# Kernel tuning notes

Measured on AMD Instinct MI355X. Metric: run time of the kernel, lower is better.

## Reference

```python
import jax, jax.numpy as jnp
import numpy as np

N_NODES = 50000
N_EDGES = 1000000
IN_CH = 128
OUT_CH = 128
N_HEADS = 8
CIS = 8.0


def _edge_conv(x, e, wq, bq, wk, bk, wv, bv, n_heads, cis):
    """One EdgeConv layer (PyG mean aggregation, source_to_target flow)."""
    src, dst = e[0], e[1]                       # x_j = x[src], x_i = x[dst]
    xi = x[dst]
    xj = x[src]
    feat = jnp.concatenate([xi, xj - xi], axis=1)        # [E, 2C]
    q = feat @ wq + bq                                   # [E, O]
    k = feat @ wk + bk
    v = feat @ wv + bv
    E, O = q.shape
    hs = O // n_heads
    q = q.reshape(E, n_heads, hs)
    k = k.reshape(E, n_heads, hs)
    v = v.reshape(E, n_heads, hs)
    # edge_weight = sign(log|dst-src| - log(cis))
    d = jnp.abs(dst - src).astype(q.dtype)
    ew = jnp.sign(jnp.log(d) - jnp.log(jnp.asarray(cis, q.dtype)))
    v = v * ew[:, None, None]
    scale = jnp.asarray(1.0 / np.sqrt(hs), q.dtype)
    probs = jax.nn.softmax(q * k * scale, axis=-1)       # softmax over head_size
    ctx = (probs * v).reshape(E, O)                      # [E, O]
    n = x.shape[0]
    s = jax.ops.segment_sum(ctx, dst, num_segments=n)    # mean aggr over targets
    cnt = jax.ops.segment_sum(jnp.ones((E,), ctx.dtype), dst, num_segments=n)
    return s / jnp.maximum(cnt, 1.0)[:, None]


def setup_inputs() -> dict:
    key = jax.random.key(0)
    ks = jax.random.split(key, 24)
    x = jax.random.normal(ks[0], (N_NODES, IN_CH), jnp.float32)
    edge_index = jax.random.randint(ks[1], (2, N_EDGES), 0, N_NODES, dtype=jnp.int32)
    half = N_EDGES // 2
    e0 = edge_index[:, jax.random.permutation(ks[2], N_EDGES)[:half]]
    e1 = edge_index[:, jax.random.permutation(ks[3], N_EDGES)[:half]]
    e2 = edge_index[:, jax.random.permutation(ks[4], N_EDGES)[:half]]
    batch = jnp.zeros((N_NODES,), jnp.int32)

    def mk(k, i, o):
        return jax.random.normal(k, (i, o), jnp.float32) * 0.02

    def mkb(k, o):
        return jax.random.normal(k, (o,), jnp.float32) * 0.02

    # layer dims: conv0 128->128, conv1 128->64, conv2 64->128
    return dict(
        x=x, e0=e0, e1=e1, e2=e2, batch=batch,
        wq0=mk(ks[5], 2 * IN_CH, OUT_CH), bq0=mkb(ks[6], OUT_CH),
        wk0=mk(ks[7], 2 * IN_CH, OUT_CH), bk0=mkb(ks[8], OUT_CH),
        wv0=mk(ks[9], 2 * IN_CH, OUT_CH), bv0=mkb(ks[10], OUT_CH),
        wq1=mk(ks[11], 2 * OUT_CH, OUT_CH // 2), bq1=mkb(ks[12], OUT_CH // 2),
        wk1=mk(ks[13], 2 * OUT_CH, OUT_CH // 2), bk1=mkb(ks[14], OUT_CH // 2),
        wv1=mk(ks[15], 2 * OUT_CH, OUT_CH // 2), bv1=mkb(ks[16], OUT_CH // 2),
        wq2=mk(ks[17], OUT_CH, OUT_CH), bq2=mkb(ks[18], OUT_CH),
        wk2=mk(ks[19], OUT_CH, OUT_CH), bk2=mkb(ks[20], OUT_CH),
        wv2=mk(ks[21], OUT_CH, OUT_CH), bv2=mkb(ks[22], OUT_CH),
    )


def reference(x, e0, e1, e2, batch,
              wq0, bq0, wk0, bk0, wv0, bv0,
              wq1, bq1, wk1, bk1, wv1, bv1,
              wq2, bq2, wk2, bk2, wv2, bv2):
    x0 = jax.nn.relu(_edge_conv(x, e0, wq0, bq0, wk0, bk0, wv0, bv0, N_HEADS, CIS))
    h = jax.nn.relu(_edge_conv(x0, e1, wq1, bq1, wk1, bk1, wv1, bv1, N_HEADS, CIS))
    h = _edge_conv(h, e2, wq2, bq2, wk2, bk2, wv2, bv2, N_HEADS, CIS)
    return jax.nn.relu(h + x0)
```

## Files before the change

### kernel.cpp

```cpp
#include <hip/hip_runtime.h>
#include <hip/hip_fp16.h>


typedef _Float16 f16x8 __attribute__((ext_vector_type(8)));
typedef unsigned int u32x4 __attribute__((ext_vector_type(4)));
typedef float f32x4 __attribute__((ext_vector_type(4)));
typedef float f32x2 __attribute__((ext_vector_type(2)));

__device__ __forceinline__ unsigned short f2h(float f) {
  __half h = __float2half(f);
  return *reinterpret_cast<unsigned short*>(&h);
}
__device__ __forceinline__ __half2 ash2(unsigned w) {
  return *reinterpret_cast<__half2*>(&w);
}

__device__ __forceinline__ void pack_w_seg(const float* __restrict__ wq,
                                           const float* __restrict__ wk,
                                           const float* __restrict__ wv,
                                           unsigned short* __restrict__ dst,
                                           int IN, int O, float kscale, int id) {
  int kchunks = IN >> 5, nchunks = O >> 4;
  int total = 6 * nchunks * kchunks * 64;
  if (id >= total) return;
  int lane = id & 63;
  int frag = id >> 6;
  int kc = frag % kchunks;
  int nc = (frag / kchunks) % nchunks;
  int mat = frag / (kchunks * nchunks);
  const float* w = (mat % 3 == 0) ? wq : (mat % 3 == 1) ? wk : wv;
  float mul = (mat % 3 == 1) ? kscale : 1.0f;
  int n = nc * 16 + (lane & 15);
  int k0 = kc * 32 + (lane >> 4) * 8;
  unsigned short tmp[8];
#pragma unroll
  for (int j = 0; j < 8; ++j) {
    int row = k0 + j;
    float bot = w[(size_t)(IN + row) * O + n];
    float val = (mat < 3) ? (w[(size_t)row * O + n] - bot) : bot;
    tmp[j] = f2h(val * mul);
  }
  uint4 o;
  o.x = (unsigned)tmp[0] | ((unsigned)tmp[1] << 16);
  o.y = (unsigned)tmp[2] | ((unsigned)tmp[3] << 16);
  o.z = (unsigned)tmp[4] | ((unsigned)tmp[5] << 16);
  o.w = (unsigned)tmp[6] | ((unsigned)tmp[7] << 16);
  reinterpret_cast<uint4*>(dst)[id] = o;
}

__device__ __forceinline__ void pack_b_seg(const float* __restrict__ bq,
                                           const float* __restrict__ bk,
                                           const float* __restrict__ bv, float kscale, int O,
                                           float* __restrict__ out, int i) {
  int mat = i / O, c = i % O;
  float v = 0.f;
  if (mat == 0) v = bq[c];
  else if (mat == 1) v = bk[c] * kscale;
  else if (mat == 2) v = bv[c];
  out[i] = v;
}

__global__ void preproc(
    const int* __restrict__ e0, const int* __restrict__ e1, const int* __restrict__ e2,
    int E, int* __restrict__ hist, int* __restrict__ rank, int NP,
    const float* __restrict__ x, unsigned short* __restrict__ xb, int n8,
    const float* __restrict__ wq0, const float* __restrict__ wk0, const float* __restrict__ wv0,
    const float* __restrict__ wq1, const float* __restrict__ wk1, const float* __restrict__ wv1,
    const float* __restrict__ wq2, const float* __restrict__ wk2, const float* __restrict__ wv2,
    unsigned short* __restrict__ wp0, unsigned short* __restrict__ wp1,
    unsigned short* __restrict__ wp2,
    const float* __restrict__ bq0, const float* __restrict__ bk0, const float* __restrict__ bv0,
    const float* __restrict__ bq1, const float* __restrict__ bk1, const float* __restrict__ bv1,
    const float* __restrict__ bq2, const float* __restrict__ bk2, const float* __restrict__ bv2,
    float* __restrict__ bias0, float* __restrict__ bias1, float* __restrict__ bias2,
    float sc16, float sc8) {
  const int tid = blockIdx.x * blockDim.x + threadIdx.x;
  const int stride = gridDim.x * blockDim.x;

  for (int i = tid; i < E; i += stride) {
    rank[i] = atomicAdd(&hist[e0[E + i]], 1);
    rank[(size_t)E + i] = atomicAdd(&hist[NP + e1[E + i]], 1);
    rank[2 * (size_t)E + i] = atomicAdd(&hist[2 * NP + e2[E + i]], 1);
  }

  for (int j = tid; j < n8; j += stride) {
    float4 a = reinterpret_cast<const float4*>(x)[2 * j];
    float4 b = reinterpret_cast<const float4*>(x)[2 * j + 1];
    uint4 o;
    o.x = (unsigned)f2h(a.x) | ((unsigned)f2h(a.y) << 16);
    o.y = (unsigned)f2h(a.z) | ((unsigned)f2h(a.w) << 16);
    o.z = (unsigned)f2h(b.x) | ((unsigned)f2h(b.y) << 16);
    o.w = (unsigned)f2h(b.z) | ((unsigned)f2h(b.w) << 16);
    reinterpret_cast<uint4*>(xb)[j] = o;
  }
  if (tid < 12288) pack_w_seg(wq0, wk0, wv0, wp0, 128, 128, sc16, tid);
  else if (tid < 18432) pack_w_seg(wq1, wk1, wv1, wp1, 128, 64, sc8, tid - 12288);
  else if (tid < 24576) pack_w_seg(wq2, wk2, wv2, wp2, 64, 128, sc16, tid - 18432);
  else if (tid < 24576 + 1920) {
    int i = tid - 24576;
    if (i < 768) pack_b_seg(bq0, bk0, bv0, sc16, 128, bias0, i);
    else if (i < 1152) pack_b_seg(bq1, bk1, bv1, sc8, 64, bias1, i - 768);
    else pack_b_seg(bq2, bk2, bv2, sc16, 128, bias2, i - 1152);
  }
}

__device__ __forceinline__ int block_scan_excl256(int v, int* buf, int t, int* total) {
  buf[t] = v;
  __syncthreads();
#pragma unroll
  for (int off = 1; off < 256; off <<= 1) {
    int add = (t >= off) ? buf[t - off] : 0;
    __syncthreads();
    buf[t] += add;
    __syncthreads();
  }
  int incl = buf[t];
  *total = buf[255];
  __syncthreads();
  return incl - v;
}

__global__ void scan_pass1(const int* __restrict__ hist, int* __restrict__ excl,
                           int* __restrict__ bsum, int n, int NP) {
  __shared__ int buf[256];
  int y = blockIdx.y, t = threadIdx.x;
  int i = blockIdx.x * 256 + t;
  int v = (i < n) ? hist[y * NP + i] : 0;
  int total;
  int ex = block_scan_excl256(v, buf, t, &total);
  if (i < NP) excl[y * NP + i] = ex;
  if (t == 0) bsum[y * 256 + blockIdx.x] = total;
}

__global__ void scan_pass2(int* __restrict__ bsum, int nblk) {
  __shared__ int buf[256];
  int y = blockIdx.y, t = threadIdx.x;
  int v = (t < nblk) ? bsum[y * 256 + t] : 0;
  int total;
  int ex = block_scan_excl256(v, buf, t, &total);
  bsum[y * 256 + t] = ex;
}

__global__ void scatter3(const int* __restrict__ e0, const int* __restrict__ e1,
                         const int* __restrict__ e2, int E, const int* __restrict__ excl,
                         const int* __restrict__ bsum, const int* __restrict__ rank,
                         long long* __restrict__ pairs, int NP,
                         uint4* __restrict__ za, int na, uint4* __restrict__ zb, int nb) {
  int y = blockIdx.y;
  const int* e = (y == 0) ? e0 : (y == 1) ? e1 : e2;
  int i = blockIdx.x * 256 + threadIdx.x;
  if (i < E) {
    int sN = e[i], d = e[E + i];
    int pos = excl[y * NP + d] + bsum[y * 256 + (d >> 8)] + rank[(size_t)y * E + i];
    long long val = ((long long)(unsigned)d << 32) | (unsigned)sN;
    __builtin_nontemporal_store(val, &pairs[(size_t)y * E + pos]);
  }
  const int gid = (blockIdx.y * gridDim.x + blockIdx.x) * 256 + threadIdx.x;
  const int gstride = gridDim.x * gridDim.y * 256;
  const uint4 Z = make_uint4(0u, 0u, 0u, 0u);
  for (int j = gid; j < na; j += gstride) za[j] = Z;
  for (int j = gid; j < nb; j += gstride) zb[j] = Z;
}

template <int IN, int O, int G>
__global__ __launch_bounds__(256, 4) void node_gemm(
    const unsigned short* __restrict__ xb, int N, int NT,
    const unsigned short* __restrict__ wpack, const float* __restrict__ bias6,
    unsigned short* __restrict__ Y1, unsigned short* __restrict__ Y2) {
  constexpr int KC = IN / 32;
  constexpr int NCH = O / 16;
  constexpr int CHR = IN / 8;
  constexpr int CM = CHR - 1;
  __shared__ unsigned short tiles[64 * IN];

  const int chunk = gridDim.x >> 3;
  const int lb = (blockIdx.x & 7) * chunk + (blockIdx.x >> 3);
  if (lb >= NT * G) return;
  const int tile = lb / G;
  const int grp = lb % G;

  const int t = threadIdx.x, w = t >> 6, ln = t & 63;
  const int n0 = tile * 64;

  {
    constexpr int RPI = 64 / CHR;
    constexpr int NI = 16 / RPI;
    const int r_in = ln / CHR, c = ln % CHR;
#pragma unroll
    for (int i = 0; i < NI; ++i) {
      int row = w * 16 + i * RPI + r_in;
      int node = min(n0 + row, N - 1);
      int sc = c ^ (row & CM);
      const unsigned short* g = xb + (size_t)node * IN + sc * 8;
      unsigned short* l = &tiles[(size_t)(w * 16 + i * RPI) * IN];
      __builtin_amdgcn_global_load_lds(
          (const __attribute__((address_space(1))) unsigned int*)g,
          (__attribute__((address_space(3))) unsigned int*)l, 16, 0, 0);
    }
  }
  __syncthreads();

  const int col = ln & 15, quad = ln >> 4;
  const int g0 = grp * 8 + w * 2;

  f32x4 acc[2][4];
#pragma unroll
  for (int cc = 0; cc < 2; ++cc)
#pragma unroll
    for (int m = 0; m < 4; ++m) acc[cc][m] = (f32x4){0.f, 0.f, 0.f, 0.f};

#pragma unroll
  for (int kc = 0; kc < KC; ++kc) {
    f16x8 a[4];
#pragma unroll
    for (int m = 0; m < 4; ++m) {
      int row = m * 16 + col;
      int sc = (kc * 4 + quad) ^ (row & CM);
      a[m] = *reinterpret_cast<const f16x8*>(&tiles[(size_t)row * IN + sc * 8]);
    }
#pragma unroll
    for (int cc = 0; cc < 2; ++cc) {
      const f16x8 b = *reinterpret_cast<const f16x8*>(
          wpack + ((size_t)((g0 + cc) * KC + kc) * 64 + ln) * 8);
#pragma unroll
      for (int m = 0; m < 4; ++m)
        acc[cc][m] = __builtin_amdgcn_mfma_f32_16x16x32_f16(a[m], b, acc[cc][m], 0, 0, 0);
    }
  }

#pragma unroll
  for (int cc = 0; cc < 2; ++cc) {
    int gch = g0 + cc;
    int mat = gch / NCH, ncg = gch % NCH;
    unsigned short* Yp = (mat < 3) ? Y1 : Y2;
    int mo = (mat < 3) ? mat : mat - 3;
    float bv = bias6[gch * 16 + col];
    size_t coloff = (size_t)mo * O + ncg * 16 + col;
#pragma unroll
    for (int m = 0; m < 4; ++m)
#pragma unroll
      for (int r = 0; r < 4; ++r) {
        int node = n0 + m * 16 + quad * 4 + r;
        if (node < N) Yp[(size_t)node * (3 * O) + coloff] = f2h(acc[cc][m][r] + bv);
      }
  }
}

template <int O, int HS>
__global__ __launch_bounds__(512, 6) void edge_attn_kernel(
    const unsigned short* __restrict__ Y1, const unsigned short* __restrict__ Y2,
    const int2* __restrict__ pairs, const int E, float* __restrict__ s) {
  constexpr int NL = HS / 8;
  constexpr int PM = O / 4 - 1;
  __shared__ float ctx[64 * O];
  __shared__ int dstL[64];

  const int chunkB = gridDim.x >> 3;
  const int lb = (blockIdx.x & 7) * chunkB + (blockIdx.x >> 3);
  if (lb * 64 >= E) return;

  const int t = threadIdx.x;
  const int e = t >> 3, head = t & 7;
  const int eG = lb * 64 + e;
  const int eC = min(eG, E - 1);
  const bool valid = eG < E;
  const int2 p = pairs[eC];
  const int sN = p.x, dN = p.y;
  if ((t & 7) == 0) dstL[e] = dN;
  const float dd = fabsf((float)(dN - sN));
  const float ew = (dd > 8.f) ? 1.f : ((dd == 8.f) ? 0.f : -1.f);

  const unsigned short* b1 = Y1 + (size_t)dN * (3 * O) + head * HS;
  const unsigned short* b2 = Y2 + (size_t)sN * (3 * O) + head * HS;

  u32x4 q1[NL], q2[NL], k1[NL], k2[NL], v1[NL], v2[NL];
#pragma unroll
  for (int l = 0; l < NL; ++l) {
    q1[l] = *reinterpret_cast<const u32x4*>(b1 + l * 8);
    q2[l] = *reinterpret_cast<const u32x4*>(b2 + l * 8);
    k1[l] = *reinterpret_cast<const u32x4*>(b1 + O + l * 8);
    k2[l] = *reinterpret_cast<const u32x4*>(b2 + O + l * 8);
    v1[l] = *reinterpret_cast<const u32x4*>(b1 + 2 * O + l * 8);
    v2[l] = *reinterpret_cast<const u32x4*>(b2 + 2 * O + l * 8);
  }

  f32x2 ex2[NL * 4];
  f32x2 sum2 = (f32x2){0.f, 0.f};
#pragma unroll
  for (int l = 0; l < NL; ++l)
#pragma unroll
    for (int d = 0; d < 4; ++d) {
      __half2 qh = __hadd2(ash2(q1[l][d]), ash2(q2[l][d]));
      __half2 kh = __hadd2(ash2(k1[l][d]), ash2(k2[l][d]));
      __half2 qk = __hmul2(qh, kh);
      f32x2 eo;
      eo.x = exp2f(__low2float(qk));
      eo.y = exp2f(__high2float(qk));
      ex2[l * 4 + d] = eo;
      sum2 += eo;
    }
  const float sum = sum2.x + sum2.y;
  const float rs = valid ? (ew / sum) : 0.f;
  const f32x2 rs2 = (f32x2){rs, rs};
#pragma unroll
  for (int l = 0; l < NL; ++l) {
#pragma unroll
    for (int g2 = 0; g2 < 2; ++g2) {
      __half2 va = __hadd2(ash2(v1[l][g2 * 2]), ash2(v2[l][g2 * 2]));
      __half2 vb = __hadd2(ash2(v1[l][g2 * 2 + 1]), ash2(v2[l][g2 * 2 + 1]));
      f32x2 vva = (f32x2){__low2float(va), __high2float(va)};
      f32x2 vvb = (f32x2){__low2float(vb), __high2float(vb)};
      f32x2 oa = ex2[l * 4 + g2 * 2] * rs2 * vva;
      f32x2 ob = ex2[l * 4 + g2 * 2 + 1] * rs2 * vvb;
      f32x4 o = (f32x4){oa.x, oa.y, ob.x, ob.y};
      int g = l * 2 + g2;
      int pch = (g * 8 + head + e) & PM;
      *reinterpret_cast<f32x4*>(&ctx[e * O + pch * 4]) = o;
    }
  }
  __syncthreads();

  {
    constexpr int GRP = 512 / O;
    constexpr int EPT = 64 / GRP;
    const int hs2 = t & 7;
    const int cs = (t >> 3) & (HS - 1);
    const int colA = hs2 * HS + cs;
    const int seg0 = (t / O) * EPT;
    const int inv = (cs >> 2) * 8 + hs2;
    const int js = cs & 3;
    float run = 0.f;
    int runstart = 0;
    int dcur = dstL[seg0];
#pragma unroll
    for (int i = 0; i < EPT; ++i) {
      int ee = seg0 + i;
      int pch = (inv + ee) & PM;
      run += ctx[ee * O + pch * 4 + js];
      int dnext = (i < EPT - 1) ? dstL[ee + 1] : -1;
      if (dnext != dcur) {
        float* addr = &s[(size_t)dcur * O + colA];
        if (runstart > 0 && i < EPT - 1) *addr = run;
        else atomicAdd(addr, run);
        run = 0.f;
        runstart = i + 1;
        dcur = dnext;
      }
    }
  }
}

__global__ void finalize_relu_f32h(float* __restrict__ s, const int* __restrict__ cnt,
                                   unsigned short* __restrict__ xbo, int total4, int Odiv4) {
  int i = blockIdx.x * blockDim.x + threadIdx.x;
  if (i >= total4) return;
  int node = i / Odiv4;
  float c = fmaxf((float)cnt[node], 1.0f);
  float4 v = reinterpret_cast<float4*>(s)[i];
  v.x = fmaxf(v.x / c, 0.f);
  v.y = fmaxf(v.y / c, 0.f);
  v.z = fmaxf(v.z / c, 0.f);
  v.w = fmaxf(v.w / c, 0.f);
  reinterpret_cast<float4*>(s)[i] = v;
  ushort4 o = make_ushort4(f2h(v.x), f2h(v.y), f2h(v.z), f2h(v.w));
  reinterpret_cast<ushort4*>(xbo)[i] = o;
}

__global__ void finalize_relu_h(const float* __restrict__ s, const int* __restrict__ cnt,
                                unsigned short* __restrict__ xbo, int total4, int Odiv4) {
  int i = blockIdx.x * blockDim.x + threadIdx.x;
  if (i >= total4) return;
  int node = i / Odiv4;
  float c = fmaxf((float)cnt[node], 1.0f);
  float4 v = reinterpret_cast<const float4*>(s)[i];
  ushort4 o = make_ushort4(f2h(fmaxf(v.x / c, 0.f)), f2h(fmaxf(v.y / c, 0.f)),
                           f2h(fmaxf(v.z / c, 0.f)), f2h(fmaxf(v.w / c, 0.f)));
  reinterpret_cast<ushort4*>(xbo)[i] = o;
}

__global__ void finalize_add_relu(float* __restrict__ out, const float* __restrict__ x0,
                                  const int* __restrict__ cnt, int total4, int Odiv4) {
  int i = blockIdx.x * blockDim.x + threadIdx.x;
  if (i >= total4) return;
  int node = i / Odiv4;
  float c = fmaxf((float)cnt[node], 1.0f);
  float4 v = reinterpret_cast<float4*>(out)[i];
  float4 r = reinterpret_cast<const float4*>(x0)[i];
  v.x = fmaxf(v.x / c + r.x, 0.f);
  v.y = fmaxf(v.y / c + r.y, 0.f);
  v.z = fmaxf(v.z / c + r.z, 0.f);
  v.w = fmaxf(v.w / c + r.w, 0.f);
  reinterpret_cast<float4*>(out)[i] = v;
}

extern "C" void kernel_launch(void* const* d_in, const int* in_sizes, int n_in,
                              void* d_out, int out_size, void* d_ws, size_t ws_size,
                              hipStream_t stream) {
  const float* x = (const float*)d_in[0];
  const int* e0 = (const int*)d_in[1];
  const int* e1 = (const int*)d_in[2];
  const int* e2 = (const int*)d_in[3];
  const float* wq0 = (const float*)d_in[5];
  const float* bq0 = (const float*)d_in[6];
  const float* wk0 = (const float*)d_in[7];
  const float* bk0 = (const float*)d_in[8];
  const float* wv0 = (const float*)d_in[9];
  const float* bv0 = (const float*)d_in[10];
  const float* wq1 = (const float*)d_in[11];
  const float* bq1 = (const float*)d_in[12];
  const float* wk1 = (const float*)d_in[13];
  const float* bk1 = (const float*)d_in[14];
  const float* wv1 = (const float*)d_in[15];
  const float* bv1 = (const float*)d_in[16];
  const float* wq2 = (const float*)d_in[17];
  const float* bq2 = (const float*)d_in[18];
  const float* wk2 = (const float*)d_in[19];
  const float* bk2 = (const float*)d_in[20];
  const float* wv2 = (const float*)d_in[21];
  const float* bv2 = (const float*)d_in[22];

  const int N = in_sizes[0] / 128;
  const int E = in_sizes[1] / 2;
  const int NBLK = (N + 255) / 256;
  const int NP = NBLK * 256;
  const float LOG2E = 1.4426950408889634f;
  const float SC16 = 0.25f * LOG2E;
  const float SC8 = 0.35355339059327373f * LOG2E;

  unsigned short* wp0 = (unsigned short*)d_ws;
  unsigned short* wp1 = wp0 + 98304;
  unsigned short* wp2 = wp1 + 49152;
  float* bias0 = (float*)(wp2 + 49152);
  float* bias1 = bias0 + 768;
  float* bias2 = bias1 + 384;
  unsigned short* xb = (unsigned short*)(bias2 + 768);
  unsigned short* Y1 = xb + (size_t)N * 128;
  unsigned short* Y2 = Y1 + (size_t)N * 384;
  float* s0 = (float*)(Y2 + (size_t)N * 384);
  float* s1 = s0 + (size_t)N * 128;
  int* hist = (int*)(s1 + (size_t)N * 64);
  int* excl = hist + 3 * (size_t)NP;
  int* bsum = excl + 3 * (size_t)NP;
  int* rank = bsum + 768;
  long long* pairs = (long long*)(rank + 3 * (size_t)E + 2);

  hipMemsetAsync(hist, 0, 3 * (size_t)NP * sizeof(int), stream);

  preproc<<<2048, 256, 0, stream>>>(
      e0, e1, e2, E, hist, rank, NP,
      x, xb, N * 16,
      wq0, wk0, wv0, wq1, wk1, wv1, wq2, wk2, wv2, wp0, wp1, wp2,
      bq0, bk0, bv0, bq1, bk1, bv1, bq2, bk2, bv2, bias0, bias1, bias2,
      SC16, SC8);

  scan_pass1<<<dim3(NBLK, 3), 256, 0, stream>>>(hist, excl, bsum, N, NP);
  scan_pass2<<<dim3(1, 3), 256, 0, stream>>>(bsum, NBLK);

  const int EB256 = (E + 255) / 256;
  scatter3<<<dim3(EB256, 3), 256, 0, stream>>>(e0, e1, e2, E, excl, bsum, rank, pairs, NP,
                                               (uint4*)s0, N * 48, (uint4*)d_out, out_size / 4);

  const int NT = (N + 63) / 64;
  const int EBK = (E + 63) / 64;
  const int EGRID = 8 * ((EBK + 7) / 8);
  const int GG6 = 8 * ((NT * 6 + 7) / 8);
  const int GG3 = 8 * ((NT * 3 + 7) / 8);

  node_gemm<128, 128, 6><<<GG6, 256, 0, stream>>>(xb, N, NT, wp0, bias0, Y1, Y2);
  edge_attn_kernel<128, 16><<<EGRID, 512, 0, stream>>>(Y1, Y2, (const int2*)pairs, E, s0);
  finalize_relu_f32h<<<(N * 32 + 255) / 256, 256, 0, stream>>>(s0, hist, xb, N * 32, 32);
  node_gemm<128, 64, 3><<<GG3, 256, 0, stream>>>(xb, N, NT, wp1, bias1, Y1, Y2);
  edge_attn_kernel<64, 8><<<EGRID, 512, 0, stream>>>(Y1, Y2, (const int2*)(pairs + E), E, s1);
  finalize_relu_h<<<(N * 16 + 255) / 256, 256, 0, stream>>>(s1, hist + NP, xb, N * 16, 16);
  node_gemm<64, 128, 6><<<GG6, 256, 0, stream>>>(xb, N, NT, wp2, bias2, Y1, Y2);
  edge_attn_kernel<128, 16><<<EGRID, 512, 0, stream>>>(Y1, Y2, (const int2*)(pairs + 2 * (size_t)E),
                                                       E, (float*)d_out);
  finalize_add_relu<<<(N * 32 + 255) / 256, 256, 0, stream>>>((float*)d_out, s0, hist + 2 * NP,
                                                              N * 32, 32);
}
```

Baseline: 514.6 us.

## Fold mean-count division into edge kernel and process two edge tiles per block

The edge attention kernel now divides each edge's contribution by its destination's in-degree before accumulating, so the finalize kernels no longer read the count array or divide. Each block also handles two 64-edge tiles in a loop, halving the grid and adding a barrier between tiles. In exchange the kernel does an extra gather of the count per edge, and fewer blocks may reduce latency hiding. Rounding changes slightly because the division happens per edge instead of after summation.

```diff
diff --git a/kernel.cpp b/kernel.cpp
--- a/kernel.cpp
+++ b/kernel.cpp
@@ -249,7 +249,8 @@
 template <int O, int HS>
 __global__ __launch_bounds__(512, 6) void edge_attn_kernel(
     const unsigned short* __restrict__ Y1, const unsigned short* __restrict__ Y2,
-    const int2* __restrict__ pairs, const int E, float* __restrict__ s) {
+    const int2* __restrict__ pairs, const int E, const int* __restrict__ cnt,
+    float* __restrict__ s) {
   constexpr int NL = HS / 8;
   constexpr int PM = O / 4 - 1;
   __shared__ float ctx[64 * O];
@@ -257,139 +258,140 @@
 
   const int chunkB = gridDim.x >> 3;
   const int lb = (blockIdx.x & 7) * chunkB + (blockIdx.x >> 3);
-  if (lb * 64 >= E) return;
-
   const int t = threadIdx.x;
   const int e = t >> 3, head = t & 7;
-  const int eG = lb * 64 + e;
-  const int eC = min(eG, E - 1);
-  const bool valid = eG < E;
-  const int2 p = pairs[eC];
-  const int sN = p.x, dN = p.y;
-  if ((t & 7) == 0) dstL[e] = dN;
-  const float dd = fabsf((float)(dN - sN));
-  const float ew = (dd > 8.f) ? 1.f : ((dd == 8.f) ? 0.f : -1.f);
-
-  const unsigned short* b1 = Y1 + (size_t)dN * (3 * O) + head * HS;
-  const unsigned short* b2 = Y2 + (size_t)sN * (3 * O) + head * HS;
-
-  u32x4 q1[NL], q2[NL], k1[NL], k2[NL], v1[NL], v2[NL];
-#pragma unroll
-  for (int l = 0; l < NL; ++l) {
-    q1[l] = *reinterpret_cast<const u32x4*>(b1 + l * 8);
-    q2[l] = *reinterpret_cast<const u32x4*>(b2 + l * 8);
-    k1[l] = *reinterpret_cast<const u32x4*>(b1 + O + l * 8);
-    k2[l] = *reinterpret_cast<const u32x4*>(b2 + O + l * 8);
-    v1[l] = *reinterpret_cast<const u32x4*>(b1 + 2 * O + l * 8);
-    v2[l] = *reinterpret_cast<const u32x4*>(b2 + 2 * O + l * 8);
-  }
-
-  f32x2 ex2[NL * 4];
-  f32x2 sum2 = (f32x2){0.f, 0.f};
-#pragma unroll
-  for (int l = 0; l < NL; ++l)
-#pragma unroll
-    for (int d = 0; d < 4; ++d) {
-      __half2 qh = __hadd2(ash2(q1[l][d]), ash2(q2[l][d]));
-      __half2 kh = __hadd2(ash2(k1[l][d]), ash2(k2[l][d]));
-      __half2 qk = __hmul2(qh, kh);
-      f32x2 eo;
-      eo.x = exp2f(__low2float(qk));
-      eo.y = exp2f(__high2float(qk));
-      ex2[l * 4 + d] = eo;
-      sum2 += eo;
-    }
-  const float sum = sum2.x + sum2.y;
-  const float rs = valid ? (ew / sum) : 0.f;
-  const f32x2 rs2 = (f32x2){rs, rs};
-#pragma unroll
-  for (int l = 0; l < NL; ++l) {
-#pragma unroll
-    for (int g2 = 0; g2 < 2; ++g2) {
-      __half2 va = __hadd2(ash2(v1[l][g2 * 2]), ash2(v2[l][g2 * 2]));
-      __half2 vb = __hadd2(ash2(v1[l][g2 * 2 + 1]), ash2(v2[l][g2 * 2 + 1]));
-      f32x2 vva = (f32x2){__low2float(va), __high2float(va)};
-      f32x2 vvb = (f32x2){__low2float(vb), __high2float(vb)};
-      f32x2 oa = ex2[l * 4 + g2 * 2] * rs2 * vva;
-      f32x2 ob = ex2[l * 4 + g2 * 2 + 1] * rs2 * vvb;
-      f32x4 o = (f32x4){oa.x, oa.y, ob.x, ob.y};
-      int g = l * 2 + g2;
-      int pch = (g * 8 + head + e) & PM;
-      *reinterpret_cast<f32x4*>(&ctx[e * O + pch * 4]) = o;
-    }
-  }
-  __syncthreads();
-
-  {
-    constexpr int GRP = 512 / O;
-    constexpr int EPT = 64 / GRP;
-    const int hs2 = t & 7;
-    const int cs = (t >> 3) & (HS - 1);
-    const int colA = hs2 * HS + cs;
-    const int seg0 = (t / O) * EPT;
-    const int inv = (cs >> 2) * 8 + hs2;
-    const int js = cs & 3;
-    float run = 0.f;
-    int runstart = 0;
-    int dcur = dstL[seg0];
-#pragma unroll
-    for (int i = 0; i < EPT; ++i) {
-      int ee = seg0 + i;
-      int pch = (inv + ee) & PM;
-      run += ctx[ee * O + pch * 4 + js];
-      int dnext = (i < EPT - 1) ? dstL[ee + 1] : -1;
-      if (dnext != dcur) {
-        float* addr = &s[(size_t)dcur * O + colA];
-        if (runstart > 0 && i < EPT - 1) *addr = run;
-        else atomicAdd(addr, run);
-        run = 0.f;
-        runstart = i + 1;
-        dcur = dnext;
+
+#pragma unroll 1
+  for (int it = 0; it < 2; ++it) {
+    const int lg = lb * 2 + it;
+    if (lg * 64 >= E) break;
+    if (it) __syncthreads();
+
+    const int eG = lg * 64 + e;
+    const int eC = min(eG, E - 1);
+    const bool valid = eG < E;
+    const int2 p = pairs[eC];
+    const int sN = p.x, dN = p.y;
+    if ((t & 7) == 0) dstL[e] = dN;
+    const float dd = fabsf((float)(dN - sN));
+    const float ew = (dd > 8.f) ? 1.f : ((dd == 8.f) ? 0.f : -1.f);
+    const float cn = (float)cnt[dN];
+
+    const unsigned short* b1 = Y1 + (size_t)dN * (3 * O) + head * HS;
+    const unsigned short* b2 = Y2 + (size_t)sN * (3 * O) + head * HS;
+
+    u32x4 q1[NL], q2[NL], k1[NL], k2[NL], v1[NL], v2[NL];
+#pragma unroll
+    for (int l = 0; l < NL; ++l) {
+      q1[l] = *reinterpret_cast<const u32x4*>(b1 + l * 8);
+      q2[l] = *reinterpret_cast<const u32x4*>(b2 + l * 8);
+      k1[l] = *reinterpret_cast<const u32x4*>(b1 + O + l * 8);
+      k2[l] = *reinterpret_cast<const u32x4*>(b2 + O + l * 8);
+      v1[l] = *reinterpret_cast<const u32x4*>(b1 + 2 * O + l * 8);
+      v2[l] = *reinterpret_cast<const u32x4*>(b2 + 2 * O + l * 8);
+    }
+
+    f32x2 ex2[NL * 4];
+    f32x2 sum2 = (f32x2){0.f, 0.f};
+#pragma unroll
+    for (int l = 0; l < NL; ++l)
+#pragma unroll
+      for (int d = 0; d < 4; ++d) {
+        __half2 qh = __hadd2(ash2(q1[l][d]), ash2(q2[l][d]));
+        __half2 kh = __hadd2(ash2(k1[l][d]), ash2(k2[l][d]));
+        __half2 qk = __hmul2(qh, kh);
+        f32x2 eo;
+        eo.x = exp2f(__low2float(qk));
+        eo.y = exp2f(__high2float(qk));
+        ex2[l * 4 + d] = eo;
+        sum2 += eo;
       }
-    }
-  }
-}
-
-__global__ void finalize_relu_f32h(float* __restrict__ s, const int* __restrict__ cnt,
-                                   unsigned short* __restrict__ xbo, int total4, int Odiv4) {
+    const float sum = sum2.x + sum2.y;
+    const float rs = valid ? (ew / (sum * cn)) : 0.f;
+    const f32x2 rs2 = (f32x2){rs, rs};
+#pragma unroll
+    for (int l = 0; l < NL; ++l) {
+#pragma unroll
+      for (int g2 = 0; g2 < 2; ++g2) {
+        __half2 va = __hadd2(ash2(v1[l][g2 * 2]), ash2(v2[l][g2 * 2]));
+        __half2 vb = __hadd2(ash2(v1[l][g2 * 2 + 1]), ash2(v2[l][g2 * 2 + 1]));
+        f32x2 vva = (f32x2){__low2float(va), __high2float(va)};
+        f32x2 vvb = (f32x2){__low2float(vb), __high2float(vb)};
+        f32x2 oa = ex2[l * 4 + g2 * 2] * rs2 * vva;
+        f32x2 ob = ex2[l * 4 + g2 * 2 + 1] * rs2 * vvb;
+        f32x4 o = (f32x4){oa.x, oa.y, ob.x, ob.y};
+        int g = l * 2 + g2;
+        int pch = (g * 8 + head + e) & PM;
+        *reinterpret_cast<f32x4*>(&ctx[e * O + pch * 4]) = o;
+      }
+    }
+    __syncthreads();
+
+    {
+      constexpr int GRP = 512 / O;
+      constexpr int EPT = 64 / GRP;
+      const int hs2 = t & 7;
+      const int cs = (t >> 3) & (HS - 1);
+      const int colA = hs2 * HS + cs;
+      const int seg0 = (t / O) * EPT;
+      const int inv = (cs >> 2) * 8 + hs2;
+      const int js = cs & 3;
+      float run = 0.f;
+      int runstart = 0;
+      int dcur = dstL[seg0];
+#pragma unroll
+      for (int i = 0; i < EPT; ++i) {
+        int ee = seg0 + i;
+        int pch = (inv + ee) & PM;
+        run += ctx[ee * O + pch * 4 + js];
+        int dnext = (i < EPT - 1) ? dstL[ee + 1] : -1;
+        if (dnext != dcur) {
+          float* addr = &s[(size_t)dcur * O + colA];
+          if (runstart > 0 && i < EPT - 1) *addr = run;
+          else atomicAdd(addr, run);
+          run = 0.f;
+          runstart = i + 1;
+          dcur = dnext;
+        }
+      }
+    }
+  }
+}
+
+__global__ void finalize_relu_f32h(float* __restrict__ s, unsigned short* __restrict__ xbo,
+                                   int total4) {
   int i = blockIdx.x * blockDim.x + threadIdx.x;
   if (i >= total4) return;
-  int node = i / Odiv4;
-  float c = fmaxf((float)cnt[node], 1.0f);
   float4 v = reinterpret_cast<float4*>(s)[i];
-  v.x = fmaxf(v.x / c, 0.f);
-  v.y = fmaxf(v.y / c, 0.f);
-  v.z = fmaxf(v.z / c, 0.f);
-  v.w = fmaxf(v.w / c, 0.f);
+  v.x = fmaxf(v.x, 0.f);
+  v.y = fmaxf(v.y, 0.f);
+  v.z = fmaxf(v.z, 0.f);
+  v.w = fmaxf(v.w, 0.f);
   reinterpret_cast<float4*>(s)[i] = v;
   ushort4 o = make_ushort4(f2h(v.x), f2h(v.y), f2h(v.z), f2h(v.w));
   reinterpret_cast<ushort4*>(xbo)[i] = o;
 }
 
-__global__ void finalize_relu_h(const float* __restrict__ s, const int* __restrict__ cnt,
-                                unsigned short* __restrict__ xbo, int total4, int Odiv4) {
+__global__ void finalize_relu_h(const float* __restrict__ s, unsigned short* __restrict__ xbo,
+                                int total4) {
   int i = blockIdx.x * blockDim.x + threadIdx.x;
   if (i >= total4) return;
-  int node = i / Odiv4;
-  float c = fmaxf((float)cnt[node], 1.0f);
   float4 v = reinterpret_cast<const float4*>(s)[i];
-  ushort4 o = make_ushort4(f2h(fmaxf(v.x / c, 0.f)), f2h(fmaxf(v.y / c, 0.f)),
-                           f2h(fmaxf(v.z / c, 0.f)), f2h(fmaxf(v.w / c, 0.f)));
+  ushort4 o = make_ushort4(f2h(fmaxf(v.x, 0.f)), f2h(fmaxf(v.y, 0.f)),
+                           f2h(fmaxf(v.z, 0.f)), f2h(fmaxf(v.w, 0.f)));
   reinterpret_cast<ushort4*>(xbo)[i] = o;
 }
 
 __global__ void finalize_add_relu(float* __restrict__ out, const float* __restrict__ x0,
-                                  const int* __restrict__ cnt, int total4, int Odiv4) {
+                                  int total4) {
   int i = blockIdx.x * blockDim.x + threadIdx.x;
   if (i >= total4) return;
-  int node = i / Odiv4;
-  float c = fmaxf((float)cnt[node], 1.0f);
   float4 v = reinterpret_cast<float4*>(out)[i];
   float4 r = reinterpret_cast<const float4*>(x0)[i];
-  v.x = fmaxf(v.x / c + r.x, 0.f);
-  v.y = fmaxf(v.y / c + r.y, 0.f);
-  v.z = fmaxf(v.z / c + r.z, 0.f);
-  v.w = fmaxf(v.w / c + r.w, 0.f);
+  v.x = fmaxf(v.x + r.x, 0.f);
+  v.y = fmaxf(v.y + r.y, 0.f);
+  v.z = fmaxf(v.z + r.z, 0.f);
+  v.w = fmaxf(v.w + r.w, 0.f);
   reinterpret_cast<float4*>(out)[i] = v;
 }
 
@@ -461,20 +463,21 @@
                                                (uint4*)s0, N * 48, (uint4*)d_out, out_size / 4);
 
   const int NT = (N + 63) / 64;
-  const int EBK = (E + 63) / 64;
-  const int EGRID = 8 * ((EBK + 7) / 8);
+  const int NG = (E + 63) / 64;
+  const int NB2 = (NG + 1) / 2;
+  const int EGRID = 8 * ((NB2 + 7) / 8);
   const int GG6 = 8 * ((NT * 6 + 7) / 8);
   const int GG3 = 8 * ((NT * 3 + 7) / 8);
 
   node_gemm<128, 128, 6><<<GG6, 256, 0, stream>>>(xb, N, NT, wp0, bias0, Y1, Y2);
-  edge_attn_kernel<128, 16><<<EGRID, 512, 0, stream>>>(Y1, Y2, (const int2*)pairs, E, s0);
-  finalize_relu_f32h<<<(N * 32 + 255) / 256, 256, 0, stream>>>(s0, hist, xb, N * 32, 32);
+  edge_attn_kernel<128, 16><<<EGRID, 512, 0, stream>>>(Y1, Y2, (const int2*)pairs, E, hist, s0);
+  finalize_relu_f32h<<<(N * 32 + 255) / 256, 256, 0, stream>>>(s0, xb, N * 32);
   node_gemm<128, 64, 3><<<GG3, 256, 0, stream>>>(xb, N, NT, wp1, bias1, Y1, Y2);
-  edge_attn_kernel<64, 8><<<EGRID, 512, 0, stream>>>(Y1, Y2, (const int2*)(pairs + E), E, s1);
-  finalize_relu_h<<<(N * 16 + 255) / 256, 256, 0, stream>>>(s1, hist + NP, xb, N * 16, 16);
+  edge_attn_kernel<64, 8><<<EGRID, 512, 0, stream>>>(Y1, Y2, (const int2*)(pairs + E), E,
+                                                     hist + NP, s1);
+  finalize_relu_h<<<(N * 16 + 255) / 256, 256, 0, stream>>>(s1, xb, N * 16);
   node_gemm<64, 128, 6><<<GG6, 256, 0, stream>>>(xb, N, NT, wp2, bias2, Y1, Y2);
   edge_attn_kernel<128, 16><<<EGRID, 512, 0, stream>>>(Y1, Y2, (const int2*)(pairs + 2 * (size_t)E),
-                                                       E, (float*)d_out);
-  finalize_add_relu<<<(N * 32 + 255) / 256, 256, 0, stream>>>((float*)d_out, s0, hist + 2 * NP,
-                                                              N * 32, 32);
-}
+                                                       E, hist + 2 * NP, (float*)d_out);
+  finalize_add_relu<<<(N * 32 + 255) / 256, 256, 0, stream>>>((float*)d_out, s0, N * 32);
+}
```

After: 531.1 us. +3.2%, slower.
